# Kernel tuning notes

Hardware: AMD Instinct MI355X
Metric: run time of the kernel (lower is better)

The kernel has to match this reference:

```python
import jax, jax.numpy as jnp
import numpy as np
import math

B, L, H, NL, TAG = 32, 64, 200, 2, 6   # dialogues, utterances/dialogue, hidden, GCNII layers, classes
M = 3                                   # modalities (a, v, t)
A = B * L                               # nodes per modality
N = M * A                               # total graph nodes
LAMDA, ALPHA = 0.5, 0.1


def setup_inputs() -> dict:
    key = jax.random.key(0)
    ks = jax.random.split(key, 12)
    s = lambda k, shape: jax.random.normal(k, shape, jnp.float32) * 0.05
    return {
        "x_a": jax.random.normal(ks[0], (B, L, H), jnp.float32),
        "x_v": jax.random.normal(ks[1], (B, L, H), jnp.float32),
        "x_t": jax.random.normal(ks[2], (B, L, H), jnp.float32),
        "fc0_w": s(ks[3], (H, H)),
        "fc0_b": jnp.zeros((H,), jnp.float32),
        "conv_w": s(ks[4], (NL, 2 * H, H)),
        "tm_w": s(ks[5], (M, 2 * H, H)),
        "tm_b": jnp.zeros((M, H), jnp.float32),
        "cross_w": s(ks[6], (6, 3 * H, H)),
        "cross_b": jnp.zeros((6, H), jnp.float32),
        "uni_w": s(ks[7], (M, H, TAG)),
        "uni_b": jnp.zeros((M, TAG), jnp.float32),
    }


def build_adj(feats):
    """feats: [M, A, H]; dialogues are contiguous blocks of L nodes.
    Returns symmetric-normalized [N, N] adjacency (block-diagonal per dialogue
    within each modality, diagonal cross-modal links)."""
    f = feats.reshape(M, B, L, H)
    nrm = f / jnp.linalg.norm(f, axis=-1, keepdims=True)
    # intra-modal per-dialogue cosine-similarity blocks -> angular similarity
    intra = jnp.einsum('mbih,mbjh->mbij', nrm, nrm) * 0.99999
    intra = 1.0 - jnp.arccos(intra) / jnp.pi          # [M,B,L,L]
    # cross-modal per-utterance cosine sim (diagonal entries)
    cross = jnp.einsum('mbih,nbih->mnbi', nrm, nrm) * 0.99999
    cross = 1.0 - jnp.arccos(cross) / jnp.pi          # [M,M,B,L]

    adj = jnp.zeros((N, N), jnp.float32)
    base = jnp.arange(B)[:, None] * L + jnp.arange(L)[None, :]          # [B,L]
    rows = jnp.arange(M)[:, None, None] * A + base[None]                # [M,B,L]
    # intra-modal block-diagonal placement
    adj = adj.at[rows[:, :, :, None], rows[:, :, None, :]].set(intra)
    # cross-modal diagonals (m==n entries equal intra diag, overwrite is identical)
    r = jnp.arange(M)[:, None] * A + jnp.arange(A)[None, :]             # [M,A]
    adj = adj.at[r[:, None, :], r[None, :, :]].set(cross.reshape(M, M, A))
    # symmetric degree normalization D^-1/2 A D^-1/2 (D diagonal -> scale)
    dinv = adj.sum(1) ** -0.5
    return adj * dinv[:, None] * dinv[None, :]


def gcnii(x, adj, fc0_w, fc0_b, conv_w):
    """GCNII (variant=True, use_residue=True). x: [N,H] -> [N,2H]."""
    h = jax.nn.relu(x @ fc0_w + fc0_b)
    h0 = h
    for i in range(NL):
        hi = adj @ h
        support = jnp.concatenate([hi, h0], axis=1)       # variant: [N,2H]
        r = (1.0 - ALPHA) * hi + ALPHA * h0
        beta = math.log(LAMDA / (i + 1) + 1.0)
        h = jax.nn.relu(beta * (support @ conv_w[i]) + (1.0 - beta) * r)
    return jnp.concatenate([x, h], axis=1)                # use_residue


def gated_attention(reps, tm_w, tm_b, cross_w, cross_b):
    """MMGatedAttention. reps: list of M arrays [A, 2H] -> list of M [A, H]."""
    hx = [jax.nn.relu(reps[m] @ tm_w[m] + tm_b[m]) for m in range(M)]
    out, p = [], 0
    for i in range(M):
        hi = jnp.zeros_like(hx[i])
        for j in range(M):
            if i == j:
                continue
            cat = jnp.concatenate([hx[i], hx[j], hx[i] * hx[j]], axis=-1)
            z = jax.nn.sigmoid(cat @ cross_w[p] + cross_b[p])
            hi = hi + z * hx[i] + (1.0 - z) * hx[j]
            p += 1
        out.append(hi)
    return out


def reference(x_a, x_v, x_t, fc0_w, fc0_b, conv_w, tm_w, tm_b,
              cross_w, cross_b, uni_w, uni_b):
    feats = jnp.stack([x_a.reshape(A, H), x_v.reshape(A, H), x_t.reshape(A, H)])  # [M,A,H]
    adj = build_adj(feats)
    big = feats.reshape(N, H)
    g = gcnii(big, adj, fc0_w, fc0_b, conv_w)                 # [N,2H]
    reps = [g[m * A:(m + 1) * A] for m in range(M)]
    h = gated_attention(reps, tm_w, tm_b, cross_w, cross_b)   # M x [A,H]
    logits = [h[m] @ uni_w[m] + uni_b[m] for m in range(M)]
    joint = logits[0] + logits[1] + logits[2]                 # [A, TAG]
    return joint
```

## Files before the change

### kernel.cpp

```cpp
#include <hip/hip_runtime.h>
#include <math.h>

#define H 200
constexpr float INV_PI = 0.31830988618379067f;

typedef __attribute__((ext_vector_type(8))) short bf16x8;
typedef __attribute__((ext_vector_type(4))) float f32x4;
typedef __attribute__((ext_vector_type(4))) short s16x4;

__device__ __forceinline__ short f2bf(float f) {
  unsigned u = __float_as_uint(f);
  u += 0x7FFF + ((u >> 16) & 1);
  return (short)(u >> 16);
}
__device__ __forceinline__ float bf2f(short s) {
  return __uint_as_float(((unsigned)(unsigned short)s) << 16);
}
__device__ __forceinline__ float angsim(float c) {
  c = fminf(fmaxf(c * 0.99999f, -1.f), 1.f);
  return 1.f - acosf(c) * INV_PI;
}
__device__ __forceinline__ const float* sel_mod(int m, const float* xa, const float* xv,
                                                const float* xt) {
  return (m == 0) ? xa : ((m == 1) ? xv : xt);
}

template <int NK>
__device__ __forceinline__ void gemm1(const short* __restrict__ A, int lda,
                                      const short* __restrict__ B, int ldb, f32x4& acc) {
  const int l = threadIdx.x & 63;
  const short* ap = A + (l & 15) * lda + (l >> 4) * 8;
  const short* bp = B + (l & 15) * ldb + (l >> 4) * 8;
  #pragma unroll
  for (int t = 0; t < NK; t++) {
    bf16x8 a = *(const bf16x8*)(ap + t * 32);
    bf16x8 b = *(const bf16x8*)(bp + t * 32);
    acc = __builtin_amdgcn_mfma_f32_16x16x32_bf16(a, b, acc, 0, 0, 0);
  }
}

template <int NK>
__device__ __forceinline__ void gemm4(const short* __restrict__ A, int lda,
                                      const short* __restrict__ B, int ldb, f32x4 acc[4]) {
  const int l = threadIdx.x & 63;
  const short* ap = A + (l & 15) * lda + (l >> 4) * 8;
  const short* bp = B + (l & 15) * ldb + (l >> 4) * 8;
  const int o16 = 16 * ldb, o32 = 32 * ldb, o48 = 48 * ldb;
  #pragma unroll
  for (int t = 0; t < NK; t++) {
    bf16x8 a = *(const bf16x8*)(ap + t * 32);
    bf16x8 b0 = *(const bf16x8*)(bp + t * 32);
    bf16x8 b1 = *(const bf16x8*)(bp + o16 + t * 32);
    bf16x8 b2 = *(const bf16x8*)(bp + o32 + t * 32);
    bf16x8 b3 = *(const bf16x8*)(bp + o48 + t * 32);
    acc[0] = __builtin_amdgcn_mfma_f32_16x16x32_bf16(a, b0, acc[0], 0, 0, 0);
    acc[1] = __builtin_amdgcn_mfma_f32_16x16x32_bf16(a, b1, acc[1], 0, 0, 0);
    acc[2] = __builtin_amdgcn_mfma_f32_16x16x32_bf16(a, b2, acc[2], 0, 0, 0);
    acc[3] = __builtin_amdgcn_mfma_f32_16x16x32_bf16(a, b3, acc[3], 0, 0, 0);
  }
}

__global__ __launch_bounds__(256) void pre_k(
    const float* __restrict__ xa, const float* __restrict__ xv, const float* __restrict__ xt,
    const float* __restrict__ fc0_w, const float* __restrict__ conv_w,
    const float* __restrict__ tm_w, const float* __restrict__ cross_w,
    short* __restrict__ fc0_wt, short* __restrict__ conv_wt, short* __restrict__ tm_wt,
    short* __restrict__ cross_wt, short* __restrict__ bigA, short* __restrict__ tmA,
    short* __restrict__ convA, short* __restrict__ hxb,
    float* __restrict__ inv_norm, float* __restrict__ cw) {
  const int lane = threadIdx.x & 63;
  const int wid = blockIdx.x * 4 + (threadIdx.x >> 6);

  if (wid < 6144) {
    int u = wid, m = u >> 11, a = u & 2047;
    const float* p = sel_mod(m, xa, xv, xt) + a * H;
    float v0 = p[lane], v1 = p[lane + 64], v2 = p[lane + 128];
    float v3 = (lane < 8) ? p[lane + 192] : 0.f;
    float s = v0 * v0 + v1 * v1 + v2 * v2 + v3 * v3;
    #pragma unroll
    for (int off = 32; off; off >>= 1) s += __shfl_down(s, off, 64);
    if (lane == 0) inv_norm[u] = 1.f / sqrtf(s);
    short b0 = f2bf(v0), b1 = f2bf(v1), b2 = f2bf(v2), b3 = f2bf(v3);
    short* br = bigA + u * 224;
    br[lane] = b0; br[lane + 64] = b1; br[lane + 128] = b2;
    if (lane < 32) br[192 + lane] = (lane < 8) ? b3 : (short)0;
    short* tr = tmA + u * 416;
    tr[lane] = b0; tr[lane + 64] = b1; tr[lane + 128] = b2;
    if (lane < 8) tr[192 + lane] = b3;
    if (lane < 16) { tr[400 + lane] = 0; convA[u * 416 + 400 + lane] = 0; }
    if (lane < 24) hxb[u * 224 + 200 + lane] = 0;
  } else if (wid < 8192) {
    int a = wid - 6144;
    const float* pa = xa + a * H;
    const float* pv = xv + a * H;
    const float* pt = xt + a * H;
    float a0 = pa[lane], a1 = pa[lane + 64], a2 = pa[lane + 128],
          a3 = (lane < 8) ? pa[lane + 192] : 0.f;
    float q0 = pv[lane], q1 = pv[lane + 64], q2 = pv[lane + 128],
          q3 = (lane < 8) ? pv[lane + 192] : 0.f;
    float t0 = pt[lane], t1 = pt[lane + 64], t2 = pt[lane + 128],
          t3 = (lane < 8) ? pt[lane + 192] : 0.f;
    float red[6];
    red[0] = a0 * a0 + a1 * a1 + a2 * a2 + a3 * a3;
    red[1] = q0 * q0 + q1 * q1 + q2 * q2 + q3 * q3;
    red[2] = t0 * t0 + t1 * t1 + t2 * t2 + t3 * t3;
    red[3] = a0 * q0 + a1 * q1 + a2 * q2 + a3 * q3;
    red[4] = a0 * t0 + a1 * t1 + a2 * t2 + a3 * t3;
    red[5] = q0 * t0 + q1 * t1 + q2 * t2 + q3 * t3;
    #pragma unroll
    for (int off = 32; off; off >>= 1)
      #pragma unroll
      for (int q = 0; q < 6; q++) red[q] += __shfl_down(red[q], off, 64);
    if (lane == 0) {
      float ia = 1.f / sqrtf(red[0]), iv = 1.f / sqrtf(red[1]), it = 1.f / sqrtf(red[2]);
      cw[a] = angsim(red[3] * ia * iv);
      cw[2048 + a] = angsim(red[4] * ia * it);
      cw[4096 + a] = angsim(red[5] * iv * it);
    }
  }

  const int S0 = 208 * 224, S1 = 208 * 416, S2 = 3 * 208 * 224;
  const int totalW = S0 + 5 * S1 + 6 * S2;
  for (int idx = blockIdx.x * 256 + threadIdx.x; idx < totalW; idx += gridDim.x * 256) {
    if (idx < S0) {
      int c = idx / 224, k = idx - c * 224;
      fc0_wt[idx] = (k < 200 && c < 200) ? f2bf(fc0_w[k * 200 + c]) : (short)0;
    } else if (idx < S0 + 5 * S1) {
      int rem = idx - S0;
      int b = rem / S1; rem -= b * S1;
      int c = rem / 416, k = rem - c * 416;
      const float* src; short* dst;
      if (b < 2) { src = conv_w + b * 80000; dst = conv_wt + b * S1; }
      else { src = tm_w + (b - 2) * 80000; dst = tm_wt + (b - 2) * S1; }
      dst[c * 416 + k] = (k < 400 && c < 200) ? f2bf(src[k * 200 + c]) : (short)0;
    } else {
      int rem = idx - S0 - 5 * S1;
      int p = rem / S2; rem -= p * S2;
      int ph = rem / (208 * 224); rem -= ph * (208 * 224);
      int c = rem / 224, k = rem - c * 224;
      cross_wt[((p * 3 + ph) * 208 + c) * 224 + k] =
          (k < 200 && c < 200) ? f2bf(cross_w[p * 120000 + (ph * 200 + k) * 200 + c]) : (short)0;
    }
  }
}

__global__ __launch_bounds__(256) void intra_g_k(const short* __restrict__ bigA,
    const float* __restrict__ inv_norm, const float* __restrict__ cw,
    short* __restrict__ intra_b, float* __restrict__ dinv) {
  const int mb = blockIdx.x, w = threadIdx.x >> 6;
  f32x4 acc[4] = {};
  gemm4<7>(bigA + (mb * 64 + w * 16) * 224, 224, bigA + mb * 64 * 224, 224, acc);
  const int l = threadIdx.x & 63, fr = l & 15, fq = l >> 4;
  const int iL0 = w * 16 + fq * 4, u0 = mb * 64;
  float rsum[4] = {0.f, 0.f, 0.f, 0.f};
  #pragma unroll
  for (int j = 0; j < 4; j++) {
    int jn = j * 16 + fr;
    float invj = inv_norm[u0 + jn];
    #pragma unroll
    for (int r = 0; r < 4; r++) {
      float ang = angsim(acc[j][r] * inv_norm[u0 + iL0 + r] * invj);
      intra_b[mb * 4096 + (iL0 + r) * 64 + jn] = f2bf(ang);
      rsum[r] += ang;
    }
  }
  #pragma unroll
  for (int mask = 1; mask < 16; mask <<= 1)
    #pragma unroll
    for (int r = 0; r < 4; r++) rsum[r] += __shfl_xor(rsum[r], mask, 64);
  if (fr == 0) {
    int m = u0 >> 11;
    #pragma unroll
    for (int r = 0; r < 4; r++) {
      int u = u0 + iL0 + r, a = u & 2047;
      float c1 = (m <= 1) ? cw[a] : cw[2048 + a];
      float c2 = (m == 0) ? cw[2048 + a] : cw[4096 + a];
      dinv[u] = 1.f / sqrtf(rsum[r] + c1 + c2);
    }
  }
}

__global__ __launch_bounds__(256) void fc0_g_k(const short* __restrict__ fc0_wt,
    const short* __restrict__ bigA, const float* __restrict__ bias,
    const float* __restrict__ dinv, short* __restrict__ convA, short* __restrict__ hs_t) {
  const int w = threadIdx.x >> 6;
  const int c0 = blockIdx.y * 16;
  const int n0 = (blockIdx.x * 4 + w) * 16;
  f32x4 acc = {};
  gemm1<7>(fc0_wt + c0 * 224, 224, bigA + n0 * 224, 224, acc);
  const int l = threadIdx.x & 63;
  const int node = n0 + (l & 15), cb = c0 + (l >> 4) * 4;
  if (cb >= 200) return;
  float dv = dinv[node];
  s16x4 oh;
  #pragma unroll
  for (int r = 0; r < 4; r++) {
    float v = fmaxf(acc[r] + bias[cb + r], 0.f);
    oh[r] = f2bf(v);
    hs_t[(cb + r) * 6144 + node] = f2bf(v * dv);
  }
  *(s16x4*)(convA + node * 416 + 200 + cb) = oh;
}

__global__ __launch_bounds__(256) void adj_g_k(const short* __restrict__ hs_t,
    const short* __restrict__ intra_b, const float* __restrict__ cw,
    const float* __restrict__ dinv, short* __restrict__ convA) {
  const int mb = blockIdx.x, w = threadIdx.x >> 6;
  const int c0 = blockIdx.y * 16;
  const int nbase = mb * 64, ug = w * 16;
  f32x4 acc = {};
  gemm1<2>(hs_t + c0 * 6144 + nbase, 6144, intra_b + mb * 4096 + ug * 64, 64, acc);
  const int l = threadIdx.x & 63;
  const int u = nbase + ug + (l & 15), cb = c0 + (l >> 4) * 4;
  if (cb >= 200) return;
  const int m = u >> 11, a = u & 2047;
  int n1, n2, p1, p2;
  if (m == 0)      { n1 = 1; p1 = 0; n2 = 2; p2 = 1; }
  else if (m == 1) { n1 = 0; p1 = 0; n2 = 2; p2 = 2; }
  else             { n1 = 0; p1 = 1; n2 = 1; p2 = 2; }
  float w1 = cw[p1 * 2048 + a], w2 = cw[p2 * 2048 + a];
  float dv = dinv[u];
  int o1 = n1 * 2048 + a, o2 = n2 * 2048 + a;
  s16x4 o;
  #pragma unroll
  for (int r = 0; r < 4; r++) {
    int c = cb + r;
    float v = dv * (acc[r] + w1 * bf2f(hs_t[c * 6144 + o1]) + w2 * bf2f(hs_t[c * 6144 + o2]));
    o[r] = f2bf(v);
  }
  *(s16x4*)(convA + u * 416 + cb) = o;
}

__global__ __launch_bounds__(256) void conv_g_k(const short* __restrict__ Wt,
    const short* __restrict__ convA, const float* __restrict__ dinv, float beta,
    int writeHs, short* __restrict__ hs_t, short* __restrict__ tmA) {
  const int w = threadIdx.x >> 6;
  const int c0 = blockIdx.y * 16;
  const int n0 = (blockIdx.x * 4 + w) * 16;
  f32x4 acc = {};
  gemm1<13>(Wt + c0 * 416, 416, convA + n0 * 416, 416, acc);
  const int l = threadIdx.x & 63;
  const int node = n0 + (l & 15), cb = c0 + (l >> 4) * 4;
  if (cb >= 200) return;
  s16x4 hiv = *(const s16x4*)(convA + node * 416 + cb);
  s16x4 h0v = *(const s16x4*)(convA + node * 416 + 200 + cb);
  float ombeta = 1.f - beta;
  if (writeHs) {
    float dv = dinv[node];
    #pragma unroll
    for (int r = 0; r < 4; r++) {
      float rr = 0.9f * bf2f(hiv[r]) + 0.1f * bf2f(h0v[r]);
      float v = fmaxf(beta * acc[r] + ombeta * rr, 0.f);
      hs_t[(cb + r) * 6144 + node] = f2bf(v * dv);
    }
  } else {
    s16x4 o;
    #pragma unroll
    for (int r = 0; r < 4; r++) {
      float rr = 0.9f * bf2f(hiv[r]) + 0.1f * bf2f(h0v[r]);
      float v = fmaxf(beta * acc[r] + ombeta * rr, 0.f);
      o[r] = f2bf(v);
    }
    *(s16x4*)(tmA + node * 416 + 200 + cb) = o;
  }
}

__global__ __launch_bounds__(256) void tm_g_k(const short* __restrict__ tm_wt,
    const short* __restrict__ tmA, const float* __restrict__ tmb, short* __restrict__ hxb) {
  const int m = blockIdx.z, w = threadIdx.x >> 6;
  const int c0 = blockIdx.y * 16;
  const int n0 = (blockIdx.x * 4 + w) * 16;
  f32x4 acc = {};
  gemm1<13>(tm_wt + m * (208 * 416) + c0 * 416, 416, tmA + (m * 2048 + n0) * 416, 416, acc);
  const int l = threadIdx.x & 63;
  const int node = n0 + (l & 15), cb = c0 + (l >> 4) * 4;
  if (cb >= 200) return;
  s16x4 o;
  #pragma unroll
  for (int r = 0; r < 4; r++) o[r] = f2bf(fmaxf(acc[r] + tmb[m * H + cb + r], 0.f));
  *(s16x4*)(hxb + (m * 2048 + node) * 224 + cb) = o;
}

__global__ __launch_bounds__(256) void crossg_g_k(const short* __restrict__ cross_wt,
    const short* __restrict__ hxb, const float* __restrict__ cb_,
    const float* __restrict__ uniw, const float* __restrict__ unib, float* __restrict__ out) {
  const int jm_t[6] = {1, 2, 0, 2, 0, 1};
  const int p = blockIdx.z, w = threadIdx.x >> 6;
  const int im = p >> 1, jm = jm_t[p];
  const int c0 = blockIdx.y * 16;
  const int n0 = (blockIdx.x * 4 + w) * 16;
  const short* Wp = cross_wt + p * (3 * 208 * 224);
  const short* Bi = hxb + (im * 2048 + n0) * 224;
  const short* Bj = hxb + (jm * 2048 + n0) * 224;
  f32x4 acc = {};
  gemm1<7>(Wp + c0 * 224, 224, Bi, 224, acc);
  gemm1<7>(Wp + 208 * 224 + c0 * 224, 224, Bj, 224, acc);
  {
    const int l = threadIdx.x & 63;
    const short* ap = Wp + 2 * 208 * 224 + (c0 + (l & 15)) * 224 + (l >> 4) * 8;
    const short* bpi = Bi + (l & 15) * 224 + (l >> 4) * 8;
    const short* bpj = Bj + (l & 15) * 224 + (l >> 4) * 8;
    #pragma unroll
    for (int t = 0; t < 7; t++) {
      bf16x8 a = *(const bf16x8*)(ap + t * 32);
      bf16x8 bi = *(const bf16x8*)(bpi + t * 32);
      bf16x8 bj = *(const bf16x8*)(bpj + t * 32);
      bf16x8 pr;
      #pragma unroll
      for (int e = 0; e < 8; e++) pr[e] = f2bf(bf2f(bi[e]) * bf2f(bj[e]));
      acc = __builtin_amdgcn_mfma_f32_16x16x32_bf16(a, pr, acc, 0, 0, 0);
    }
  }
  const int l = threadIdx.x & 63;
  const int node = n0 + (l & 15), cb = c0 + (l >> 4) * 4;
  float pt[6] = {0.f, 0.f, 0.f, 0.f, 0.f, 0.f};
  if (cb < 200) {
    s16x4 ai = *(const s16x4*)(hxb + (im * 2048 + node) * 224 + cb);
    s16x4 aj = *(const s16x4*)(hxb + (jm * 2048 + node) * 224 + cb);
    const float* Wu = uniw + im * (H * 6);
    #pragma unroll
    for (int r = 0; r < 4; r++) {
      float x = acc[r] + cb_[p * H + cb + r];
      float z = 1.f / (1.f + expf(-x));
      float o = z * bf2f(ai[r]) + (1.f - z) * bf2f(aj[r]);
      #pragma unroll
      for (int t = 0; t < 6; t++) pt[t] += o * Wu[(cb + r) * 6 + t];
    }
  }
  #pragma unroll
  for (int t = 0; t < 6; t++) {
    pt[t] += __shfl_xor(pt[t], 16, 64);
    pt[t] += __shfl_xor(pt[t], 32, 64);
  }
  if ((l >> 4) == 0) {
    if (p == 0 && blockIdx.y == 0) {
      #pragma unroll
      for (int t = 0; t < 6; t++) pt[t] += unib[t] + unib[6 + t] + unib[12 + t];
    }
    #pragma unroll
    for (int t = 0; t < 6; t++) atomicAdd(out + node * 6 + t, pt[t]);
  }
}

extern "C" void kernel_launch(void* const* d_in, const int* in_sizes, int n_in,
                              void* d_out, int out_size, void* d_ws, size_t ws_size,
                              hipStream_t stream) {
  const float* xa = (const float*)d_in[0];
  const float* xv = (const float*)d_in[1];
  const float* xt = (const float*)d_in[2];
  const float* fc0_w = (const float*)d_in[3];
  const float* fc0_b = (const float*)d_in[4];
  const float* conv_w = (const float*)d_in[5];
  const float* tm_w = (const float*)d_in[6];
  const float* tm_b = (const float*)d_in[7];
  const float* cross_w = (const float*)d_in[8];
  const float* cross_b = (const float*)d_in[9];
  const float* uni_w = (const float*)d_in[10];
  const float* uni_b = (const float*)d_in[11];
  float* out = (float*)d_out;
  float* ws = (float*)d_ws;

  float* inv_norm = ws;
  float* dinv = ws + 6144;
  float* cw = ws + 12288;
  short* bigA = (short*)(ws + 18432);
  short* convA = (short*)(ws + 706560);
  short* tmA = (short*)(ws + 1984512);
  short* hxb = (short*)(ws + 3262464);
  short* hs_t = (short*)(ws + 3950592);
  short* intra_b = (short*)(ws + 4589568);
  short* fc0_wt = (short*)(ws + 4786176);
  short* conv_wt = (short*)(ws + 4809472);
  short* tm_wt = (short*)(ws + 4896000);
  short* cross_wt = (short*)(ws + 5025792);

  hipMemsetAsync(out, 0, (size_t)out_size * sizeof(float), stream);
  pre_k<<<2048, 256, 0, stream>>>(xa, xv, xt, fc0_w, conv_w, tm_w, cross_w,
                                  fc0_wt, conv_wt, tm_wt, cross_wt,
                                  bigA, tmA, convA, hxb, inv_norm, cw);
  intra_g_k<<<96, 256, 0, stream>>>(bigA, inv_norm, cw, intra_b, dinv);
  fc0_g_k<<<dim3(96, 13), 256, 0, stream>>>(fc0_wt, bigA, fc0_b, dinv, convA, hs_t);
  adj_g_k<<<dim3(96, 13), 256, 0, stream>>>(hs_t, intra_b, cw, dinv, convA);
  conv_g_k<<<dim3(96, 13), 256, 0, stream>>>(conv_wt, convA, dinv,
                                             0.40546510810816444f, 1, hs_t, tmA);
  adj_g_k<<<dim3(96, 13), 256, 0, stream>>>(hs_t, intra_b, cw, dinv, convA);
  conv_g_k<<<dim3(96, 13), 256, 0, stream>>>(conv_wt + 208 * 416, convA, dinv,
                                             0.22314355131420976f, 0, hs_t, tmA);
  tm_g_k<<<dim3(32, 13, 3), 256, 0, stream>>>(tm_wt, tmA, tm_b, hxb);
  crossg_g_k<<<dim3(32, 13, 6), 256, 0, stream>>>(cross_wt, hxb, cross_b, uni_w, uni_b, out);
}
```

Measured before the change: 177.6 us.

## Tile weight transposes in LDS, fold memset into pre_k, merge intra and fc0 kernels

```diff
diff --git a/kernel.cpp b/kernel.cpp
--- a/kernel.cpp
+++ b/kernel.cpp
@@ -67,12 +67,41 @@
     short* __restrict__ fc0_wt, short* __restrict__ conv_wt, short* __restrict__ tm_wt,
     short* __restrict__ cross_wt, short* __restrict__ bigA, short* __restrict__ tmA,
     short* __restrict__ convA, short* __restrict__ hxb,
-    float* __restrict__ inv_norm, float* __restrict__ cw) {
+    float* __restrict__ inv_norm, float* __restrict__ cw, float* __restrict__ out) {
+  __shared__ float tile[64][65];
+  const int bx = blockIdx.x;
   const int lane = threadIdx.x & 63;
-  const int wid = blockIdx.x * 4 + (threadIdx.x >> 6);
-
-  if (wid < 6144) {
-    int u = wid, m = u >> 11, a = u & 2047;
+  const int wrp = threadIdx.x >> 6;
+
+  if (bx < 444) {
+    const float* src; short* dst; int srcK, KP, kt, ct;
+    if (bx < 16) {
+      src = fc0_w; dst = fc0_wt; srcK = 200; KP = 224; kt = bx >> 2; ct = bx & 3;
+    } else if (bx < 156) {
+      int b = (bx - 16) / 28, rem = (bx - 16) % 28;
+      kt = rem >> 2; ct = rem & 3; srcK = 400; KP = 416;
+      if (b < 2) { src = conv_w + b * 80000; dst = conv_wt + b * 86528; }
+      else { src = tm_w + (b - 2) * 80000; dst = tm_wt + (b - 2) * 86528; }
+    } else {
+      int q = bx - 156, pp = q >> 4, rem = q & 15;
+      kt = rem >> 2; ct = rem & 3; srcK = 200; KP = 224;
+      src = cross_w + (pp / 3) * 120000 + (pp % 3) * 40000;
+      dst = cross_wt + pp * (208 * 224);
+    }
+    const int k0 = kt * 64, c0 = ct * 64;
+    #pragma unroll 4
+    for (int r = 0; r < 16; r++) {
+      int ky = r * 4 + wrp, k = k0 + ky, c = c0 + lane;
+      tile[ky][lane] = (k < srcK && c < 200) ? src[k * 200 + c] : 0.f;
+    }
+    __syncthreads();
+    #pragma unroll 4
+    for (int r = 0; r < 16; r++) {
+      int cy = r * 4 + wrp, c = c0 + cy, k = k0 + lane;
+      if (c < 208 && k < KP) dst[c * KP + k] = f2bf(tile[lane][cy]);
+    }
+  } else if (bx < 1980) {
+    int u = (bx - 444) * 4 + wrp, m = u >> 11, a = u & 2047;
     const float* p = sel_mod(m, xa, xv, xt) + a * H;
     float v0 = p[lane], v1 = p[lane + 64], v2 = p[lane + 128];
     float v3 = (lane < 8) ? p[lane + 192] : 0.f;
@@ -89,8 +118,8 @@
     if (lane < 8) tr[192 + lane] = b3;
     if (lane < 16) { tr[400 + lane] = 0; convA[u * 416 + 400 + lane] = 0; }
     if (lane < 24) hxb[u * 224 + 200 + lane] = 0;
-  } else if (wid < 8192) {
-    int a = wid - 6144;
+  } else if (bx < 2492) {
+    int a = (bx - 1980) * 4 + wrp;
     const float* pa = xa + a * H;
     const float* pv = xv + a * H;
     const float* pt = xt + a * H;
@@ -117,99 +146,90 @@
       cw[2048 + a] = angsim(red[4] * ia * it);
       cw[4096 + a] = angsim(red[5] * iv * it);
     }
-  }
-
-  const int S0 = 208 * 224, S1 = 208 * 416, S2 = 3 * 208 * 224;
-  const int totalW = S0 + 5 * S1 + 6 * S2;
-  for (int idx = blockIdx.x * 256 + threadIdx.x; idx < totalW; idx += gridDim.x * 256) {
-    if (idx < S0) {
-      int c = idx / 224, k = idx - c * 224;
-      fc0_wt[idx] = (k < 200 && c < 200) ? f2bf(fc0_w[k * 200 + c]) : (short)0;
-    } else if (idx < S0 + 5 * S1) {
-      int rem = idx - S0;
-      int b = rem / S1; rem -= b * S1;
-      int c = rem / 416, k = rem - c * 416;
-      const float* src; short* dst;
-      if (b < 2) { src = conv_w + b * 80000; dst = conv_wt + b * S1; }
-      else { src = tm_w + (b - 2) * 80000; dst = tm_wt + (b - 2) * S1; }
-      dst[c * 416 + k] = (k < 400 && c < 200) ? f2bf(src[k * 200 + c]) : (short)0;
-    } else {
-      int rem = idx - S0 - 5 * S1;
-      int p = rem / S2; rem -= p * S2;
-      int ph = rem / (208 * 224); rem -= ph * (208 * 224);
-      int c = rem / 224, k = rem - c * 224;
-      cross_wt[((p * 3 + ph) * 208 + c) * 224 + k] =
-          (k < 200 && c < 200) ? f2bf(cross_w[p * 120000 + (ph * 200 + k) * 200 + c]) : (short)0;
-    }
-  }
-}
-
-__global__ __launch_bounds__(256) void intra_g_k(const short* __restrict__ bigA,
+  } else {
+    int i = (bx - 2492) * 1024 + threadIdx.x * 4;
+    *(f32x4*)(out + i) = f32x4{0.f, 0.f, 0.f, 0.f};
+  }
+}
+
+__global__ __launch_bounds__(256) void intra_fc0_k(const short* __restrict__ bigA,
     const float* __restrict__ inv_norm, const float* __restrict__ cw,
-    short* __restrict__ intra_b, float* __restrict__ dinv) {
-  const int mb = blockIdx.x, w = threadIdx.x >> 6;
-  f32x4 acc[4] = {};
-  gemm4<7>(bigA + (mb * 64 + w * 16) * 224, 224, bigA + mb * 64 * 224, 224, acc);
-  const int l = threadIdx.x & 63, fr = l & 15, fq = l >> 4;
-  const int iL0 = w * 16 + fq * 4, u0 = mb * 64;
-  float rsum[4] = {0.f, 0.f, 0.f, 0.f};
-  #pragma unroll
-  for (int j = 0; j < 4; j++) {
-    int jn = j * 16 + fr;
-    float invj = inv_norm[u0 + jn];
+    const short* __restrict__ fc0_wt, const float* __restrict__ bias,
+    short* __restrict__ intra_s, float* __restrict__ dinv,
+    short* __restrict__ convA, short* __restrict__ h_t) {
+  __shared__ float sdinv[64];
+  const int l = threadIdx.x & 63;
+  const int w = threadIdx.x >> 6;
+  if (blockIdx.x < 96) {
+    const int mb = blockIdx.x;
+    f32x4 acc[4] = {};
+    gemm4<7>(bigA + (mb * 64 + w * 16) * 224, 224, bigA + mb * 64 * 224, 224, acc);
+    const int fr = l & 15, fq = l >> 4;
+    const int iL0 = w * 16 + fq * 4, u0 = mb * 64;
+    float ang[4][4];
+    float rsum[4] = {0.f, 0.f, 0.f, 0.f};
+    #pragma unroll
+    for (int j = 0; j < 4; j++) {
+      float invj = inv_norm[u0 + j * 16 + fr];
+      #pragma unroll
+      for (int r = 0; r < 4; r++) {
+        float av = angsim(acc[j][r] * inv_norm[u0 + iL0 + r] * invj);
+        ang[j][r] = av;
+        rsum[r] += av;
+      }
+    }
+    #pragma unroll
+    for (int mask = 1; mask < 16; mask <<= 1)
+      #pragma unroll
+      for (int r = 0; r < 4; r++) rsum[r] += __shfl_xor(rsum[r], mask, 64);
+    if (fr == 0) {
+      int m = u0 >> 11;
+      #pragma unroll
+      for (int r = 0; r < 4; r++) {
+        int u = u0 + iL0 + r, a = u & 2047;
+        float c1 = (m <= 1) ? cw[a] : cw[2048 + a];
+        float c2 = (m == 0) ? cw[2048 + a] : cw[4096 + a];
+        float dv = 1.f / sqrtf(rsum[r] + c1 + c2);
+        dinv[u] = dv;
+        sdinv[iL0 + r] = dv;
+      }
+    }
+    __syncthreads();
+    #pragma unroll
+    for (int j = 0; j < 4; j++) {
+      int jn = j * 16 + fr;
+      float dj = sdinv[jn];
+      #pragma unroll
+      for (int r = 0; r < 4; r++)
+        intra_s[mb * 4096 + (iL0 + r) * 64 + jn] = f2bf(ang[j][r] * sdinv[iL0 + r] * dj);
+    }
+  } else {
+    const int bx2 = blockIdx.x - 96;
+    const int c0 = (bx2 / 96) * 16;
+    const int n0 = ((bx2 % 96) * 4 + w) * 16;
+    f32x4 acc = {};
+    gemm1<7>(fc0_wt + c0 * 224, 224, bigA + n0 * 224, 224, acc);
+    const int node = n0 + (l & 15), cb = c0 + (l >> 4) * 4;
+    if (cb >= 200) return;
+    s16x4 oh;
     #pragma unroll
     for (int r = 0; r < 4; r++) {
-      float ang = angsim(acc[j][r] * inv_norm[u0 + iL0 + r] * invj);
-      intra_b[mb * 4096 + (iL0 + r) * 64 + jn] = f2bf(ang);
-      rsum[r] += ang;
-    }
-  }
-  #pragma unroll
-  for (int mask = 1; mask < 16; mask <<= 1)
-    #pragma unroll
-    for (int r = 0; r < 4; r++) rsum[r] += __shfl_xor(rsum[r], mask, 64);
-  if (fr == 0) {
-    int m = u0 >> 11;
-    #pragma unroll
-    for (int r = 0; r < 4; r++) {
-      int u = u0 + iL0 + r, a = u & 2047;
-      float c1 = (m <= 1) ? cw[a] : cw[2048 + a];
-      float c2 = (m == 0) ? cw[2048 + a] : cw[4096 + a];
-      dinv[u] = 1.f / sqrtf(rsum[r] + c1 + c2);
-    }
-  }
-}
-
-__global__ __launch_bounds__(256) void fc0_g_k(const short* __restrict__ fc0_wt,
-    const short* __restrict__ bigA, const float* __restrict__ bias,
-    const float* __restrict__ dinv, short* __restrict__ convA, short* __restrict__ hs_t) {
-  const int w = threadIdx.x >> 6;
-  const int c0 = blockIdx.y * 16;
-  const int n0 = (blockIdx.x * 4 + w) * 16;
-  f32x4 acc = {};
-  gemm1<7>(fc0_wt + c0 * 224, 224, bigA + n0 * 224, 224, acc);
-  const int l = threadIdx.x & 63;
-  const int node = n0 + (l & 15), cb = c0 + (l >> 4) * 4;
-  if (cb >= 200) return;
-  float dv = dinv[node];
-  s16x4 oh;
-  #pragma unroll
-  for (int r = 0; r < 4; r++) {
-    float v = fmaxf(acc[r] + bias[cb + r], 0.f);
-    oh[r] = f2bf(v);
-    hs_t[(cb + r) * 6144 + node] = f2bf(v * dv);
-  }
-  *(s16x4*)(convA + node * 416 + 200 + cb) = oh;
-}
-
-__global__ __launch_bounds__(256) void adj_g_k(const short* __restrict__ hs_t,
-    const short* __restrict__ intra_b, const float* __restrict__ cw,
+      float v = fmaxf(acc[r] + bias[cb + r], 0.f);
+      oh[r] = f2bf(v);
+      h_t[(cb + r) * 6144 + node] = oh[r];
+    }
+    *(s16x4*)(convA + node * 416 + 200 + cb) = oh;
+  }
+}
+
+__global__ __launch_bounds__(256) void adj_g_k(const short* __restrict__ h_t,
+    const short* __restrict__ intra_s, const float* __restrict__ cw,
     const float* __restrict__ dinv, short* __restrict__ convA) {
   const int mb = blockIdx.x, w = threadIdx.x >> 6;
   const int c0 = blockIdx.y * 16;
   const int nbase = mb * 64, ug = w * 16;
   f32x4 acc = {};
-  gemm1<2>(hs_t + c0 * 6144 + nbase, 6144, intra_b + mb * 4096 + ug * 64, 64, acc);
+  gemm1<2>(h_t + c0 * 6144 + nbase, 6144, intra_s + mb * 4096 + ug * 64, 64, acc);
   const int l = threadIdx.x & 63;
   const int u = nbase + ug + (l & 15), cb = c0 + (l >> 4) * 4;
   if (cb >= 200) return;
@@ -218,22 +238,23 @@
   if (m == 0)      { n1 = 1; p1 = 0; n2 = 2; p2 = 1; }
   else if (m == 1) { n1 = 0; p1 = 0; n2 = 2; p2 = 2; }
   else             { n1 = 0; p1 = 1; n2 = 1; p2 = 2; }
-  float w1 = cw[p1 * 2048 + a], w2 = cw[p2 * 2048 + a];
   float dv = dinv[u];
   int o1 = n1 * 2048 + a, o2 = n2 * 2048 + a;
+  float w1 = cw[p1 * 2048 + a] * dv * dinv[o1];
+  float w2 = cw[p2 * 2048 + a] * dv * dinv[o2];
   s16x4 o;
   #pragma unroll
   for (int r = 0; r < 4; r++) {
     int c = cb + r;
-    float v = dv * (acc[r] + w1 * bf2f(hs_t[c * 6144 + o1]) + w2 * bf2f(hs_t[c * 6144 + o2]));
+    float v = acc[r] + w1 * bf2f(h_t[c * 6144 + o1]) + w2 * bf2f(h_t[c * 6144 + o2]);
     o[r] = f2bf(v);
   }
   *(s16x4*)(convA + u * 416 + cb) = o;
 }
 
 __global__ __launch_bounds__(256) void conv_g_k(const short* __restrict__ Wt,
-    const short* __restrict__ convA, const float* __restrict__ dinv, float beta,
-    int writeHs, short* __restrict__ hs_t, short* __restrict__ tmA) {
+    const short* __restrict__ convA, float beta, int writeHs,
+    short* __restrict__ h_t, short* __restrict__ tmA) {
   const int w = threadIdx.x >> 6;
   const int c0 = blockIdx.y * 16;
   const int n0 = (blockIdx.x * 4 + w) * 16;
@@ -246,12 +267,11 @@
   s16x4 h0v = *(const s16x4*)(convA + node * 416 + 200 + cb);
   float ombeta = 1.f - beta;
   if (writeHs) {
-    float dv = dinv[node];
     #pragma unroll
     for (int r = 0; r < 4; r++) {
       float rr = 0.9f * bf2f(hiv[r]) + 0.1f * bf2f(h0v[r]);
       float v = fmaxf(beta * acc[r] + ombeta * rr, 0.f);
-      hs_t[(cb + r) * 6144 + node] = f2bf(v * dv);
+      h_t[(cb + r) * 6144 + node] = f2bf(v);
     }
   } else {
     s16x4 o;
@@ -367,25 +387,24 @@
   short* convA = (short*)(ws + 706560);
   short* tmA = (short*)(ws + 1984512);
   short* hxb = (short*)(ws + 3262464);
-  short* hs_t = (short*)(ws + 3950592);
-  short* intra_b = (short*)(ws + 4589568);
+  short* h_t = (short*)(ws + 3950592);
+  short* intra_s = (short*)(ws + 4589568);
   short* fc0_wt = (short*)(ws + 4786176);
   short* conv_wt = (short*)(ws + 4809472);
   short* tm_wt = (short*)(ws + 4896000);
   short* cross_wt = (short*)(ws + 5025792);
 
-  hipMemsetAsync(out, 0, (size_t)out_size * sizeof(float), stream);
-  pre_k<<<2048, 256, 0, stream>>>(xa, xv, xt, fc0_w, conv_w, tm_w, cross_w,
+  pre_k<<<2504, 256, 0, stream>>>(xa, xv, xt, fc0_w, conv_w, tm_w, cross_w,
                                   fc0_wt, conv_wt, tm_wt, cross_wt,
-                                  bigA, tmA, convA, hxb, inv_norm, cw);
-  intra_g_k<<<96, 256, 0, stream>>>(bigA, inv_norm, cw, intra_b, dinv);
-  fc0_g_k<<<dim3(96, 13), 256, 0, stream>>>(fc0_wt, bigA, fc0_b, dinv, convA, hs_t);
-  adj_g_k<<<dim3(96, 13), 256, 0, stream>>>(hs_t, intra_b, cw, dinv, convA);
-  conv_g_k<<<dim3(96, 13), 256, 0, stream>>>(conv_wt, convA, dinv,
-                                             0.40546510810816444f, 1, hs_t, tmA);
-  adj_g_k<<<dim3(96, 13), 256, 0, stream>>>(hs_t, intra_b, cw, dinv, convA);
-  conv_g_k<<<dim3(96, 13), 256, 0, stream>>>(conv_wt + 208 * 416, convA, dinv,
-                                             0.22314355131420976f, 0, hs_t, tmA);
+                                  bigA, tmA, convA, hxb, inv_norm, cw, out);
+  intra_fc0_k<<<1344, 256, 0, stream>>>(bigA, inv_norm, cw, fc0_wt, fc0_b,
+                                        intra_s, dinv, convA, h_t);
+  adj_g_k<<<dim3(96, 13), 256, 0, stream>>>(h_t, intra_s, cw, dinv, convA);
+  conv_g_k<<<dim3(96, 13), 256, 0, stream>>>(conv_wt, convA,
+                                             0.40546510810816444f, 1, h_t, tmA);
+  adj_g_k<<<dim3(96, 13), 256, 0, stream>>>(h_t, intra_s, cw, dinv, convA);
+  conv_g_k<<<dim3(96, 13), 256, 0, stream>>>(conv_wt + 208 * 416, convA,
+                                             0.22314355131420976f, 0, h_t, tmA);
   tm_g_k<<<dim3(32, 13, 3), 256, 0, stream>>>(tm_wt, tmA, tm_b, hxb);
   crossg_g_k<<<dim3(32, 13, 6), 256, 0, stream>>>(cross_wt, hxb, cross_b, uni_w, uni_b, out);
 }
```

After: 172.8 us. -2.7%, faster.
